# Kernel tuning notes

Hardware: AMD Instinct MI355X
Metric: run time of the kernel (lower is better)

## Reference

```python
import jax, jax.numpy as jnp
import numpy as np

MAX_LAG_FRACTION = 0.25


def setup_inputs() -> dict:
    key = jax.random.key(0)
    k1, k2, k3 = jax.random.split(key, 3)
    B, T, D = 64, 1024, 2
    alpha_pred = jax.random.uniform(k1, (B,), dtype=jnp.float32) * 2.0  # alpha in (0, 2)
    trajectory = jax.random.normal(k2, (B, T, D), dtype=jnp.float32)
    lengths = jax.random.randint(k3, (B,), T // 2, T + 1, dtype=jnp.int64)
    return {"alpha_pred": alpha_pred, "trajectory": trajectory, "lengths": lengths}


def reference(alpha_pred, trajectory, lengths):
    B, T, D = trajectory.shape
    max_lag = max(1, int(T * MAX_LAG_FRACTION))  # static; lags beyond length are masked
    lags_i = jnp.arange(1, max_lag + 1)                      # (L,)
    log_lags = jnp.log(lags_i.astype(jnp.float32))           # (L,)
    P = T - 1
    positions = jnp.arange(P)                                # (P,)

    end_idx = positions[None, :] + lags_i[:, None]           # (L, P)
    pos_valid = end_idx < T                                  # (L, P)
    end_c = jnp.minimum(end_idx, T - 1)

    traj_end = trajectory[:, end_c, :]                       # (B, L, P, D) gather
    traj_start = trajectory[:, :P, :][:, None, :, :]         # (B, 1, P, D)
    disp = traj_end - traj_start                             # (B, L, P, D)

    # valid if position < length - lag (and end index in-bounds)
    sample_valid = positions[None, None, :] < (lengths[:, None, None] - lags_i[None, :, None])
    valid = (pos_valid[None, :, :] & sample_valid).astype(jnp.float32)  # (B, L, P)

    sq_disp = jnp.sum(disp * disp, axis=-1)                  # (B, L, P)
    counts = jnp.maximum(jnp.sum(valid, axis=-1), 1.0)       # (B, L)
    msd = jnp.sum(sq_disp * valid, axis=-1) / counts         # (B, L)

    lag_mask = (lengths[:, None] > lags_i[None, :]).astype(jnp.float32)  # (B, L)
    log_msd = jnp.log(msd + 1e-8)                            # (B, L)

    alpha = alpha_pred[:, None]                              # (B, 1)
    resid = log_msd - alpha * log_lags[None, :]
    denom = jnp.maximum(jnp.sum(lag_mask, axis=1), 1.0)      # (B,)
    intercept = jnp.sum(resid * lag_mask, axis=1) / denom    # (B,)

    sq_err = (alpha * log_lags[None, :] + intercept[:, None] - log_msd) ** 2
    per_traj = jnp.sum(sq_err * lag_mask, axis=1) / denom
    return jnp.mean(per_traj)
```

## Files before the change

kernel.cpp:

```cpp
#include <hip/hip_runtime.h>
#include <hip/hip_bf16.h>

#define TT 1024
#define DD 2
#define MAXLAG 256
#define PCHUNKS 8
#define PCHUNK 128

__global__ __launch_bounds__(256) void msd_partial_kernel(const float* __restrict__ traj,
                                                          const int* __restrict__ lengths,
                                                          float* __restrict__ partial,
                                                          float* __restrict__ finish_ws) {
    __shared__ float s[TT * DD];
    const int b = blockIdx.x;
    const int pc = blockIdx.y;

    const float4* t4 = (const float4*)(traj + (size_t)b * TT * DD);
    float4* s4 = (float4*)s;
    for (int i = threadIdx.x; i < TT * DD / 4; i += 256) s4[i] = t4[i];

    if (b == 0 && pc == 0 && threadIdx.x < 2) finish_ws[threadIdx.x] = 0.0f;
    __syncthreads();

    const int L = lengths[b];
    const int lag = threadIdx.x + 1;
    const int cnt = L - lag;
    const int p0 = pc * PCHUNK;
    const int p1 = p0 + PCHUNK;
    const int pend = (cnt < p1) ? cnt : p1;

    const float2* s2 = (const float2*)s;
    float acc = 0.0f;
    #pragma unroll 4
    for (int p = p0; p < pend; ++p) {
        float2 a = s2[p];
        float2 e = s2[p + lag];
        float dx = e.x - a.x;
        float dy = e.y - a.y;
        acc += dx * dx + dy * dy;
    }
    partial[((size_t)b * PCHUNKS + pc) * MAXLAG + threadIdx.x] = acc;
}

__global__ __launch_bounds__(256) void fit_kernel(const float* __restrict__ alpha_pred,
                                                  const int* __restrict__ lengths,
                                                  const float* __restrict__ partial,
                                                  float* __restrict__ finish_ws,
                                                  float* __restrict__ out) {
    const int b = blockIdx.x;
    const int t = threadIdx.x;
    const int lag = t + 1;
    const int L = lengths[b];

    float acc = 0.0f;
    #pragma unroll
    for (int pc = 0; pc < PCHUNKS; ++pc)
        acc += partial[((size_t)b * PCHUNKS + pc) * MAXLAG + t];

    const float cntf = fmaxf((float)(L - lag), 1.0f);
    const float msd = acc / cntf;
    const float mask = (L > lag) ? 1.0f : 0.0f;
    const float resid = logf(msd + 1e-8f) - alpha_pred[b] * logf((float)lag);

    const int wave = t >> 6;
    const int lane = t & 63;
    __shared__ float sr[4], sm[4], ss[4];

    float r = resid * mask, mk = mask;
    for (int off = 32; off; off >>= 1) {
        r  += __shfl_down(r,  off, 64);
        mk += __shfl_down(mk, off, 64);
    }
    if (lane == 0) { sr[wave] = r; sm[wave] = mk; }
    __syncthreads();
    const float sumr  = sr[0] + sr[1] + sr[2] + sr[3];
    const float summ  = sm[0] + sm[1] + sm[2] + sm[3];
    const float denom = fmaxf(summ, 1.0f);
    const float intercept = sumr / denom;

    float d = intercept - resid;
    float se = d * d * mask;
    for (int off = 32; off; off >>= 1) se += __shfl_down(se, off, 64);
    if (lane == 0) ss[wave] = se;
    __syncthreads();

    if (t == 0) {
        const float per_traj = (ss[0] + ss[1] + ss[2] + ss[3]) / denom;
        atomicAdd(&finish_ws[0], per_traj * (1.0f / 64.0f));
        __threadfence();
        unsigned old = atomicAdd((unsigned*)&finish_ws[1], 1u);
        if (old == gridDim.x - 1)
            out[0] = *((volatile float*)&finish_ws[0]);
    }
}

extern "C" void kernel_launch(void* const* d_in, const int* in_sizes, int n_in,
                              void* d_out, int out_size, void* d_ws, size_t ws_size,
                              hipStream_t stream) {
    const float* alpha = (const float*)d_in[0];
    const float* traj  = (const float*)d_in[1];
    const int*   lens  = (const int*)d_in[2];
    float* out = (float*)d_out;

    const int B = in_sizes[0];

    float* partial   = (float*)d_ws;
    float* finish_ws = partial + (size_t)B * PCHUNKS * MAXLAG;

    dim3 g1(B, PCHUNKS);
    msd_partial_kernel<<<g1, 256, 0, stream>>>(traj, lens, partial, finish_ws);
    fit_kernel<<<B, 256, 0, stream>>>(alpha, lens, partial, finish_ws, out);
}
```

Before: 64.47 us.

## Fuse MSD and fit kernels into one cooperative launch with grid sync

```diff
diff --git a/kernel.cpp b/kernel.cpp
--- a/kernel.cpp
+++ b/kernel.cpp
@@ -1,32 +1,36 @@
 #include <hip/hip_runtime.h>
-#include <hip/hip_bf16.h>
+#include <hip/hip_cooperative_groups.h>
+
+namespace cg = cooperative_groups;
 
 #define TT 1024
 #define DD 2
 #define MAXLAG 256
-#define PCHUNKS 8
-#define PCHUNK 128
 
-__global__ __launch_bounds__(256) void msd_partial_kernel(const float* __restrict__ traj,
-                                                          const int* __restrict__ lengths,
-                                                          float* __restrict__ partial,
-                                                          float* __restrict__ finish_ws) {
+__global__ __launch_bounds__(1024) void fused_kernel(const float* __restrict__ alpha_pred,
+                                                     const float* __restrict__ traj,
+                                                     const int* __restrict__ lengths,
+                                                     float* __restrict__ ws,
+                                                     float* __restrict__ out) {
     __shared__ float s[TT * DD];
+    __shared__ float sums[4 * MAXLAG];
+    __shared__ float sr[4], sm[4], ss[4];
+
     const int b = blockIdx.x;
-    const int pc = blockIdx.y;
+    const int t = threadIdx.x;
 
     const float4* t4 = (const float4*)(traj + (size_t)b * TT * DD);
     float4* s4 = (float4*)s;
-    for (int i = threadIdx.x; i < TT * DD / 4; i += 256) s4[i] = t4[i];
-
-    if (b == 0 && pc == 0 && threadIdx.x < 2) finish_ws[threadIdx.x] = 0.0f;
+    if (t < TT * DD / 4) s4[t] = t4[t];
     __syncthreads();
 
     const int L = lengths[b];
-    const int lag = threadIdx.x + 1;
+    const int lagIdx = t & (MAXLAG - 1);
+    const int lag = lagIdx + 1;
+    const int slice = t >> 8;
     const int cnt = L - lag;
-    const int p0 = pc * PCHUNK;
-    const int p1 = p0 + PCHUNK;
+    const int p0 = slice * 256;
+    const int p1 = p0 + 256;
     const int pend = (cnt < p1) ? cnt : p1;
 
     const float2* s2 = (const float2*)s;
@@ -39,58 +43,52 @@
         float dy = e.y - a.y;
         acc += dx * dx + dy * dy;
     }
-    partial[((size_t)b * PCHUNKS + pc) * MAXLAG + threadIdx.x] = acc;
-}
+    sums[slice * MAXLAG + lagIdx] = acc;
+    __syncthreads();
 
-__global__ __launch_bounds__(256) void fit_kernel(const float* __restrict__ alpha_pred,
-                                                  const int* __restrict__ lengths,
-                                                  const float* __restrict__ partial,
-                                                  float* __restrict__ finish_ws,
-                                                  float* __restrict__ out) {
-    const int b = blockIdx.x;
-    const int t = threadIdx.x;
-    const int lag = t + 1;
-    const int L = lengths[b];
+    float resid = 0.0f, mask = 0.0f, denom = 1.0f;
+    if (t < MAXLAG) {
+        const float tot = sums[t] + sums[MAXLAG + t]
+                        + sums[2 * MAXLAG + t] + sums[3 * MAXLAG + t];
+        const float cntf = fmaxf((float)(L - lag), 1.0f);
+        const float msd = tot / cntf;
+        mask = (L > lag) ? 1.0f : 0.0f;
+        resid = logf(msd + 1e-8f) - alpha_pred[b] * logf((float)lag);
 
-    float acc = 0.0f;
-    #pragma unroll
-    for (int pc = 0; pc < PCHUNKS; ++pc)
-        acc += partial[((size_t)b * PCHUNKS + pc) * MAXLAG + t];
+        float r = resid * mask, mk = mask;
+        for (int off = 32; off; off >>= 1) {
+            r  += __shfl_down(r,  off, 64);
+            mk += __shfl_down(mk, off, 64);
+        }
+        if ((t & 63) == 0) { sr[t >> 6] = r; sm[t >> 6] = mk; }
+    }
+    __syncthreads();
 
-    const float cntf = fmaxf((float)(L - lag), 1.0f);
-    const float msd = acc / cntf;
-    const float mask = (L > lag) ? 1.0f : 0.0f;
-    const float resid = logf(msd + 1e-8f) - alpha_pred[b] * logf((float)lag);
-
-    const int wave = t >> 6;
-    const int lane = t & 63;
-    __shared__ float sr[4], sm[4], ss[4];
-
-    float r = resid * mask, mk = mask;
-    for (int off = 32; off; off >>= 1) {
-        r  += __shfl_down(r,  off, 64);
-        mk += __shfl_down(mk, off, 64);
+    if (t < MAXLAG) {
+        const float sumr = sr[0] + sr[1] + sr[2] + sr[3];
+        const float summ = sm[0] + sm[1] + sm[2] + sm[3];
+        denom = fmaxf(summ, 1.0f);
+        const float intercept = sumr / denom;
+        const float d = intercept - resid;
+        float se = d * d * mask;
+        for (int off = 32; off; off >>= 1) se += __shfl_down(se, off, 64);
+        if ((t & 63) == 0) ss[t >> 6] = se;
     }
-    if (lane == 0) { sr[wave] = r; sm[wave] = mk; }
-    __syncthreads();
-    const float sumr  = sr[0] + sr[1] + sr[2] + sr[3];
-    const float summ  = sm[0] + sm[1] + sm[2] + sm[3];
-    const float denom = fmaxf(summ, 1.0f);
-    const float intercept = sumr / denom;
-
-    float d = intercept - resid;
-    float se = d * d * mask;
-    for (int off = 32; off; off >>= 1) se += __shfl_down(se, off, 64);
-    if (lane == 0) ss[wave] = se;
     __syncthreads();
 
     if (t == 0) {
         const float per_traj = (ss[0] + ss[1] + ss[2] + ss[3]) / denom;
-        atomicAdd(&finish_ws[0], per_traj * (1.0f / 64.0f));
-        __threadfence();
-        unsigned old = atomicAdd((unsigned*)&finish_ws[1], 1u);
-        if (old == gridDim.x - 1)
-            out[0] = *((volatile float*)&finish_ws[0]);
+        __hip_atomic_store(&ws[b], per_traj, __ATOMIC_RELAXED, __HIP_MEMORY_SCOPE_AGENT);
+    }
+
+    cg::this_grid().sync();
+
+    if (b == 0 && t < 64) {
+        float v = (t < (int)gridDim.x)
+                    ? __hip_atomic_load(&ws[t], __ATOMIC_RELAXED, __HIP_MEMORY_SCOPE_AGENT)
+                    : 0.0f;
+        for (int off = 32; off; off >>= 1) v += __shfl_down(v, off, 64);
+        if (t == 0) out[0] = v / (float)gridDim.x;
     }
 }
 
@@ -101,13 +99,10 @@
     const float* traj  = (const float*)d_in[1];
     const int*   lens  = (const int*)d_in[2];
     float* out = (float*)d_out;
+    float* ws  = (float*)d_ws;
 
     const int B = in_sizes[0];
 
-    float* partial   = (float*)d_ws;
-    float* finish_ws = partial + (size_t)B * PCHUNKS * MAXLAG;
-
-    dim3 g1(B, PCHUNKS);
-    msd_partial_kernel<<<g1, 256, 0, stream>>>(traj, lens, partial, finish_ws);
-    fit_kernel<<<B, 256, 0, stream>>>(alpha, lens, partial, finish_ws, out);
+    void* args[] = { (void*)&alpha, (void*)&traj, (void*)&lens, (void*)&ws, (void*)&out };
+    hipLaunchCooperativeKernel((void*)fused_kernel, dim3(B), dim3(1024), args, 0, stream);
 }
```

After: 97.64 us. 1.51x slower.
